# Kernel optimization log

Measured on AMD Instinct MI355X. Metric: run time of the kernel, lower is better.

## Reference

```python
import jax, jax.numpy as jnp
import numpy as np

BN_EPS = 1e-5
LEAKY_SLOPE = 0.2


def setup_inputs() -> dict:
    key = jax.random.key(0)
    k1, k2 = jax.random.split(key, 2)
    B, C, N, O, K = 8, 64, 4096, 64, 20
    x = jax.random.normal(k1, (B, C, N), dtype=jnp.float32)
    W = jax.random.normal(k2, (O, 2 * C), dtype=jnp.float32) * 0.05  # 1x1 conv weight
    gamma = jnp.ones((O,), dtype=jnp.float32)
    beta = jnp.zeros((O,), dtype=jnp.float32)
    return {"x": x, "W": W, "gamma": gamma, "beta": beta, "k": K}


def reference(x, W, gamma, beta, k):
    # x: (B, C, N)
    xt = jnp.transpose(x, (0, 2, 1))  # (B, N, C)
    # kNN via squared euclidean distances (same ordering as cdist p=2)
    sq = jnp.sum(xt * xt, axis=-1)  # (B, N)
    d2 = sq[:, :, None] + sq[:, None, :] - 2.0 * jnp.einsum('bnc,bmc->bnm', xt, xt)
    idx = jax.lax.top_k(-d2, k)[1]  # (B, N, k) nearest neighbors (incl. self)
    # gather neighbor features: (B, N, k, C)
    xj = jax.vmap(lambda f, i: f[i])(xt, idx)
    xi = xt[:, :, None, :]  # (B, N, 1, C)
    edge = jnp.concatenate([xj - xi, jnp.broadcast_to(xi, xj.shape)], axis=-1)  # (B, N, k, 2C)
    # 1x1 conv == channel GEMM
    h = jnp.einsum('bnkc,oc->bnko', edge, W)  # (B, N, k, O)
    # BatchNorm2d, training-mode batch statistics over (B, N, k) per channel
    mean = jnp.mean(h, axis=(0, 1, 2))
    var = jnp.mean(jnp.square(h - mean), axis=(0, 1, 2))
    hn = (h - mean) * jax.lax.rsqrt(var + BN_EPS) * gamma + beta
    # LeakyReLU(0.2); dropout omitted (eval / identity)
    act = jnp.where(hn >= 0, hn, LEAKY_SLOPE * hn)
    # max over the k neighbors -> (B, N, O) -> (B, O, N)
    out = jnp.max(act, axis=2)
    return jnp.transpose(out, (0, 2, 1))
```

## Files before the change

### kernel.cpp

```cpp
#include <hip/hip_runtime.h>
#include <math.h>

#define Bn 8
#define Cc 64
#define Nn 4096
#define Oo 64
#define Kk 20
#define Kh 10
#define QCAP 32
#define NTOT (Bn*Nn*Kk)

typedef __attribute__((ext_vector_type(8))) short short8;
typedef __attribute__((ext_vector_type(4))) float f32x4;

__device__ __forceinline__ unsigned bf16_rn(float v) {
  unsigned u = __float_as_uint(v);
  return (u + 0x7FFFu + ((u >> 16) & 1)) >> 16;
}

__device__ __forceinline__ float pair_swap_f(float v) {
  return __int_as_float(__builtin_amdgcn_mov_dpp(__float_as_int(v), 0xB1, 0xF, 0xF, true));
}
__device__ __forceinline__ int pair_swap_i(int v) {
  return __builtin_amdgcn_mov_dpp(v, 0xB1, 0xF, 0xF, true);
}

__device__ __forceinline__ void gload_lds16(const void* g, void* l) {
  __builtin_amdgcn_global_load_lds((const __attribute__((address_space(1))) void*)g,
                                   (__attribute__((address_space(3))) void*)l,
                                   16, 0, 0);
}

__global__ __launch_bounds__(256) void k_split(const float* __restrict__ x,
                                               unsigned short* __restrict__ xs3,
                                               float* __restrict__ sqv) {
  __shared__ float xs[64][68];
  int tid = threadIdx.x;
  int b = blockIdx.x & 7;
  int n0 = (blockIdx.x >> 3) << 6;
  for (int i = 0; i < 4; i++) {
    int c = i * 16 + (tid >> 4);
    int n = (tid & 15) * 4;
    float4 v = *(const float4*)&x[((size_t)b * Cc + c) * Nn + n0 + n];
    *(float4*)&xs[c][n] = v;
  }
  __syncthreads();
  for (int i = 0; i < 4; i++) {
    int n = i * 16 + (tid >> 4);
    int c = (tid & 15) * 4;
    ushort4 h4, m4, l4;
    unsigned short* hp = (unsigned short*)&h4;
    unsigned short* mp = (unsigned short*)&m4;
    unsigned short* lp = (unsigned short*)&l4;
#pragma unroll
    for (int j = 0; j < 4; j++) {
      float v = xs[c + j][n];
      unsigned hb = bf16_rn(v);
      float hf = __uint_as_float(hb << 16);
      float r1 = v - hf;
      unsigned mb = bf16_rn(r1);
      float mf = __uint_as_float(mb << 16);
      float r2 = r1 - mf;
      unsigned lb = bf16_rn(r2);
      hp[j] = (unsigned short)hb;
      mp[j] = (unsigned short)mb;
      lp[j] = (unsigned short)lb;
    }
    size_t o = ((size_t)(b << 12) + n0 + n) * 192 + c;
    *(ushort4*)&xs3[o] = h4;
    *(ushort4*)&xs3[o + 64] = m4;
    *(ushort4*)&xs3[o + 128] = l4;
  }
  if (tid < 64) {
    float s = 0.f;
#pragma unroll
    for (int c = 0; c < 64; c++) { float v = xs[c][tid]; s = fmaf(v, v, s); }
    sqv[b * Nn + n0 + tid] = s;
  }
}

__global__ __launch_bounds__(256) void k_y1z(const float* __restrict__ x,
                                             const float* __restrict__ Wm,
                                             float* __restrict__ y1,
                                             float* __restrict__ z) {
  __shared__ float xs[64][68];
  __shared__ float Wl[64][129];
  int tid = threadIdx.x;
  int b = blockIdx.x & 7;
  int n0 = (blockIdx.x >> 3) << 6;
  for (int i = tid; i < 64 * 128; i += 256) Wl[i >> 7][i & 127] = Wm[i];
  for (int i = 0; i < 4; i++) {
    int c = i * 16 + (tid >> 4);
    int n = (tid & 15) * 4;
    float4 v = *(const float4*)&x[((size_t)b * Cc + c) * Nn + n0 + n];
    *(float4*)&xs[c][n] = v;
  }
  __syncthreads();
  int o = tid & 63, ng = tid >> 6;
  for (int p = 0; p < 4; p++) {
    int nb = p * 16 + ng * 4;
    float a1[4] = {0.f, 0.f, 0.f, 0.f};
    float a2[4] = {0.f, 0.f, 0.f, 0.f};
#pragma unroll 8
    for (int c = 0; c < 64; c++) {
      float4 xv = *(const float4*)&xs[c][nb];
      float w1v = Wl[o][c], w2v = Wl[o][64 + c];
      float xa[4] = {xv.x, xv.y, xv.z, xv.w};
#pragma unroll
      for (int j = 0; j < 4; j++) {
        a1[j] = fmaf(xa[j], w1v, a1[j]);
        a2[j] = fmaf(xa[j], w2v, a2[j]);
      }
    }
#pragma unroll
    for (int j = 0; j < 4; j++) {
      size_t off = ((size_t)b * Nn + n0 + nb + j) * 64 + o;
      y1[off] = a1[j];
      z[off] = a2[j] - a1[j];
    }
  }
}

__global__ __launch_bounds__(512, 4) void k_knn(const unsigned short* __restrict__ xs3,
                                                const float* __restrict__ sqv,
                                                int* __restrict__ idxout) {
  __shared__ alignas(16) short Bs[2][2][6144];
  __shared__ alignas(16) float thrS[2][64];
  __shared__ alignas(16) float sqs[2][2][32];
  __shared__ alignas(16) float qk[2][64][36];
  __shared__ alignas(16) unsigned short qm[2][64][40];
  __shared__ int qcnt[2][64];

  const int tid = threadIdx.x;
  const int lane = tid & 63;
  const int w = tid >> 6;
  const int grp = w >> 2;
  const int wg = w & 3;
  const int tig = tid & 255;
  const int b = blockIdx.x & 7;
  const int n0 = (blockIdx.x >> 3) << 6;
  const int lm = lane & 15;
  const int q = lane >> 4;
  const bool handler = (lane < 32);
  const int hrow = wg * 16 + (lane >> 1);
  const bool isL = (lane & 1) == 0;
  const int rowq = wg * 16 + q * 4;

  float hk[Kh];
  int hix[Kh];
#pragma unroll
  for (int kk = 0; kk < Kh; kk++) { hk[kk] = INFINITY; hix[kk] = 0; }

  if (handler && !isL) { thrS[grp][hrow] = INFINITY; qcnt[grp][hrow] = 0; }

  const size_t arow = ((size_t)(b << 12) + n0 + wg * 16 + lm) * 192;
  short8 ah0 = *(const short8*)&xs3[arow + q * 8];
  short8 ah1 = *(const short8*)&xs3[arow + 32 + q * 8];
  short8 am0 = *(const short8*)&xs3[arow + 64 + q * 8];
  short8 am1 = *(const short8*)&xs3[arow + 96 + q * 8];
  short8 al0 = *(const short8*)&xs3[arow + 128 + q * 8];
  short8 al1 = *(const short8*)&xs3[arow + 160 + q * 8];

  const unsigned short* gbase = xs3 + ((size_t)(b << 12) + grp * 2048) * 192;
  int gofs[3];
  int lofs[3];
#pragma unroll
  for (int i = 0; i < 3; i++) {
    int p = i * 256 + wg * 64 + lane;
    gofs[i] = (p ^ ((p / 24) & 7)) * 8;
    lofs[i] = (i * 256 + wg * 64) * 8;
  }
  const int qa = ((q ^ (lm & 7)) << 3);
  const int qb = (((q + 4) ^ (lm & 7)) << 3);

#pragma unroll
  for (int i = 0; i < 3; i++) gload_lds16(gbase + gofs[i], &Bs[grp][0][lofs[i]]);
  if (tig < 8) gload_lds16(sqv + b * Nn + grp * 2048 + lane * 4, &sqs[grp][0][0]);

  int cur = 0;
  for (int t = 0; t < 64; t++) {
    const int m0 = grp * 2048 + t * 32;
    __syncthreads();
    if (t < 63) {
      const unsigned short* gn = gbase + 6144;
#pragma unroll
      for (int i = 0; i < 3; i++) gload_lds16(gn + gofs[i], &Bs[grp][cur ^ 1][lofs[i]]);
      if (tig < 8) gload_lds16(sqv + b * Nn + m0 + 32 + lane * 4, &sqs[grp][cur ^ 1][0]);
      gbase = gn;
    }

    const short* Bg = &Bs[grp][cur][0];
    f32x4 acc[2];
#pragma unroll
    for (int g = 0; g < 2; g++) {
      const short* brow = Bg + (g * 16 + lm) * 192;
      short8 bh0 = *(const short8*)(brow + qa);
      short8 bh1 = *(const short8*)(brow + qb);
      short8 bm0 = *(const short8*)(brow + 64 + qa);
      short8 bm1 = *(const short8*)(brow + 64 + qb);
      short8 bl0 = *(const short8*)(brow + 128 + qa);
      short8 bl1 = *(const short8*)(brow + 128 + qb);
      f32x4 a = (f32x4){0.f, 0.f, 0.f, 0.f};
      a = __builtin_amdgcn_mfma_f32_16x16x32_bf16(am0, bm0, a, 0, 0, 0);
      a = __builtin_amdgcn_mfma_f32_16x16x32_bf16(am1, bm1, a, 0, 0, 0);
      a = __builtin_amdgcn_mfma_f32_16x16x32_bf16(ah0, bl0, a, 0, 0, 0);
      a = __builtin_amdgcn_mfma_f32_16x16x32_bf16(ah1, bl1, a, 0, 0, 0);
      a = __builtin_amdgcn_mfma_f32_16x16x32_bf16(al0, bh0, a, 0, 0, 0);
      a = __builtin_amdgcn_mfma_f32_16x16x32_bf16(al1, bh1, a, 0, 0, 0);
      a = __builtin_amdgcn_mfma_f32_16x16x32_bf16(ah0, bm0, a, 0, 0, 0);
      a = __builtin_amdgcn_mfma_f32_16x16x32_bf16(ah1, bm1, a, 0, 0, 0);
      a = __builtin_amdgcn_mfma_f32_16x16x32_bf16(am0, bh0, a, 0, 0, 0);
      a = __builtin_amdgcn_mfma_f32_16x16x32_bf16(am1, bh1, a, 0, 0, 0);
      a = __builtin_amdgcn_mfma_f32_16x16x32_bf16(ah0, bh0, a, 0, 0, 0);
      a = __builtin_amdgcn_mfma_f32_16x16x32_bf16(ah1, bh1, a, 0, 0, 0);
      acc[g] = a;
    }

    unsigned pend = 0;
    {
      float4 t4 = *(const float4*)&thrS[grp][rowq];
      float tl[4] = {t4.x, t4.y, t4.z, t4.w};
      if (grp) {
        float4 s4 = *(const float4*)&thrS[0][rowq];
        tl[0] = fminf(tl[0], s4.x); tl[1] = fminf(tl[1], s4.y);
        tl[2] = fminf(tl[2], s4.z); tl[3] = fminf(tl[3], s4.w);
      }
#pragma unroll
      for (int g = 0; g < 2; g++) {
        float sv = sqs[grp][cur][g * 16 + lm];
#pragma unroll
        for (int r = 0; r < 4; r++) {
          float key = fmaf(-2.f, acc[g][r], sv);
          acc[g][r] = key;
          if (key < tl[r]) pend |= 1u << (g * 4 + r);
        }
      }
    }

    if (pend) {
#pragma unroll
      for (int g = 0; g < 2; g++) {
#pragma unroll
        for (int r = 0; r < 4; r++) {
          unsigned bit = 1u << (g * 4 + r);
          if (pend & bit) {
            int row = rowq + r;
            int p = atomicAdd(&qcnt[grp][row], 1);
            qk[grp][row][p] = acc[g][r];
            qm[grp][row][p] = (unsigned short)(m0 + g * 16 + lm);
          }
        }
      }
    }

    if (handler) {
      int cn = qcnt[grp][hrow];
      for (int p0 = 0; p0 < cn; p0 += 2) {
        float2 kv2 = *(const float2*)&qk[grp][hrow][p0];
        ushort2 mv2 = *(const ushort2*)&qm[grp][hrow][p0];
        float kva[2] = {kv2.x, kv2.y};
        unsigned short mva[2] = {mv2.x, mv2.y};
#pragma unroll
        for (int j = 0; j < 2; j++) {
          bool valid = (p0 + j < cn);
          float kv = kva[j];
          int ki = (int)mva[j];
          bool lins = kv < hk[Kh - 1];
          float pv_ = lins ? hk[Kh - 1] : kv;
          int pi_ = lins ? hix[Kh - 1] : ki;
          float rv = pair_swap_f(pv_);
          int ri = pair_swap_i(pi_);
          float mval = isL ? kv : rv;
          int midx = isL ? ki : ri;
          if (valid && mval < hk[Kh - 1]) {
            bool cm[Kh];
#pragma unroll
            for (int kk = 0; kk < Kh; kk++) cm[kk] = mval < hk[kk];
#pragma unroll
            for (int kk = Kh - 1; kk >= 1; kk--) {
              hk[kk]  = cm[kk] ? (cm[kk - 1] ? hk[kk - 1]  : mval) : hk[kk];
              hix[kk] = cm[kk] ? (cm[kk - 1] ? hix[kk - 1] : midx) : hix[kk];
            }
            if (cm[0]) { hk[0] = mval; hix[0] = midx; }
          }
        }
      }
      if (cn && !isL) { qcnt[grp][hrow] = 0; thrS[grp][hrow] = hk[Kh - 1]; }
    }
    cur ^= 1;
  }

  if (grp == 1 && handler) {
    int base = isL ? 0 : Kh;
#pragma unroll
    for (int kk = 0; kk < Kh; kk++) {
      qk[1][hrow][base + kk] = hk[kk];
      qm[1][hrow][base + kk] = (unsigned short)hix[kk];
    }
  }
  __syncthreads();
  if (grp == 0 && handler) {
    for (int p0 = 0; p0 < Kk; p0 += 4) {
      float4 kv4 = *(const float4*)&qk[1][hrow][p0];
      ushort4 mv4 = *(const ushort4*)&qm[1][hrow][p0];
      float kva[4] = {kv4.x, kv4.y, kv4.z, kv4.w};
      unsigned short mva[4] = {mv4.x, mv4.y, mv4.z, mv4.w};
#pragma unroll
      for (int j = 0; j < 4; j++) {
        float kv = kva[j];
        int ki = (int)mva[j];
        bool lins = kv < hk[Kh - 1];
        float pv_ = lins ? hk[Kh - 1] : kv;
        int pi_ = lins ? hix[Kh - 1] : ki;
        float rv = pair_swap_f(pv_);
        int ri = pair_swap_i(pi_);
        float mval = isL ? kv : rv;
        int midx = isL ? ki : ri;
        if (mval < hk[Kh - 1]) {
          bool cm[Kh];
#pragma unroll
          for (int kk = 0; kk < Kh; kk++) cm[kk] = mval < hk[kk];
#pragma unroll
          for (int kk = Kh - 1; kk >= 1; kk--) {
            hk[kk]  = cm[kk] ? (cm[kk - 1] ? hk[kk - 1]  : mval) : hk[kk];
            hix[kk] = cm[kk] ? (cm[kk - 1] ? hix[kk - 1] : midx) : hix[kk];
          }
          if (cm[0]) { hk[0] = mval; hix[0] = midx; }
        }
      }
    }
    size_t obase = ((size_t)b * Nn + n0 + hrow) * Kk + (isL ? 0 : Kh);
#pragma unroll
    for (int kk = 0; kk < Kh; kk++) idxout[obase + kk] = hix[kk];
  }
}

__global__ __launch_bounds__(256) void k_stats(const float* __restrict__ y1,
                                               const float* __restrict__ z,
                                               const int* __restrict__ idxp,
                                               float* __restrict__ parts) {
  __shared__ float rs[4][64];
  __shared__ float rq[4][64];
  int tid = threadIdx.x;
  int o = tid & 63, g = tid >> 6;
  int b = blockIdx.x & 7;
  int n0 = (blockIdx.x >> 3) << 6;
  const float* y1b = y1 + (size_t)b * Nn * 64;
  float s = 0.f, ss = 0.f;
  for (int t = 0; t < 16; t++) {
    int n = n0 + g + t * 4;
    size_t base = (size_t)b * Nn + n;
    float zv = z[base * 64 + o];
    const int* ip = idxp + base * Kk;
#pragma unroll
    for (int k = 0; k < Kk; k++) {
      int j = ip[k];
      float hv = y1b[(size_t)j * 64 + o] + zv;
      s += hv;
      ss = fmaf(hv, hv, ss);
    }
  }
  rs[g][o] = s;
  rq[g][o] = ss;
  __syncthreads();
  if (tid < 64) {
    parts[(size_t)blockIdx.x * 128 + tid] = rs[0][tid] + rs[1][tid] + rs[2][tid] + rs[3][tid];
    parts[(size_t)blockIdx.x * 128 + 64 + tid] = rq[0][tid] + rq[1][tid] + rq[2][tid] + rq[3][tid];
  }
}

__global__ __launch_bounds__(128) void k_reduce(const float* __restrict__ parts,
                                                float* __restrict__ stats) {
  int tid = threadIdx.x;
  float s = 0.f;
  for (int i = 0; i < 512; i += 4) {
    s += parts[(size_t)i * 128 + tid] + parts[(size_t)(i + 1) * 128 + tid] +
         parts[(size_t)(i + 2) * 128 + tid] + parts[(size_t)(i + 3) * 128 + tid];
  }
  stats[tid] = s;
}

__global__ __launch_bounds__(256) void k_out(const float* __restrict__ y1,
                                             const float* __restrict__ z,
                                             const int* __restrict__ idxp,
                                             const float* __restrict__ stats,
                                             const float* __restrict__ gamma,
                                             const float* __restrict__ beta,
                                             float* __restrict__ out) {
  __shared__ float T[64][65];
  int tid = threadIdx.x;
  int lane = tid & 63;
  int w = tid >> 6;
  int b = blockIdx.x & 7;
  int n0 = (blockIdx.x >> 3) << 6;
  int o = lane;
  const float inv = 1.0f / (float)NTOT;
  float mean = stats[o] * inv;
  float var = fmaf(-mean, mean, stats[64 + o] * inv);
  float sc = gamma[o] * rsqrtf(var + 1e-5f);
  float bi = fmaf(-mean, sc, beta[o]);
  const float* y1b = y1 + (size_t)b * Nn * 64;
  for (int t = 0; t < 16; t++) {
    int nl = w + t * 4;
    size_t base = (size_t)b * Nn + n0 + nl;
    float zv = z[base * 64 + o];
    const int* ip = idxp + base * Kk;
    float mv = -INFINITY;
#pragma unroll
    for (int k = 0; k < Kk; k++) {
      int j = ip[k];
      float hv = y1b[(size_t)j * 64 + o] + zv;
      float hn = fmaf(hv, sc, bi);
      float a = (hn >= 0.f) ? hn : 0.2f * hn;
      mv = fmaxf(mv, a);
    }
    T[o][nl] = mv;
  }
  __syncthreads();
  for (int t = 0; t < 16; t++) {
    int oo = w * 16 + t;
    out[((size_t)b * Oo + oo) * Nn + n0 + lane] = T[oo][lane];
  }
}

extern "C" void kernel_launch(void* const* d_in, const int* in_sizes, int n_in,
                              void* d_out, int out_size, void* d_ws, size_t ws_size,
                              hipStream_t stream) {
  const float* x = (const float*)d_in[0];
  const float* W = (const float*)d_in[1];
  const float* gamma = (const float*)d_in[2];
  const float* beta = (const float*)d_in[3];

  char* ws = (char*)d_ws;
  unsigned short* xs3 = (unsigned short*)ws;
  float* y1 = (float*)ws;
  float* z = (float*)(ws + 8388608);
  float* sq = (float*)(ws + 16777216);
  float* stats = (float*)(ws + 16908288);
  int* idx = (int*)(ws + 16908800);
  float* parts = (float*)(ws + 19530240);
  float* out = (float*)d_out;

  k_split<<<Bn * (Nn / 64), 256, 0, stream>>>(x, xs3, sq);
  k_knn<<<Bn * (Nn / 64), 512, 0, stream>>>(xs3, sq, idx);
  k_y1z<<<Bn * (Nn / 64), 256, 0, stream>>>(x, W, y1, z);
  k_stats<<<Bn * (Nn / 64), 256, 0, stream>>>(y1, z, idx, parts);
  k_reduce<<<1, 128, 0, stream>>>(parts, stats);
  k_out<<<Bn * (Nn / 64), 256, 0, stream>>>(y1, z, idx, stats, gamma, beta, out);
}
```

Baseline: 366.6 us.

## Precompute per-point max/min of pre-BN features to avoid second neighbor gather

The stats kernel now also records the max and min of the pre-normalization feature over the k neighbors for each point and channel, writing them transposed (hmax into the output buffer, hmin into workspace). Because BN followed by LeakyReLU is monotonic in each channel (direction set by the sign of the scale), the output kernel only needs an elementwise transform of max or min instead of a second 20-way gather. The kNN candidate filter also changes: each group now tests against the other group's threshold too, with tie-breaking asymmetry, which may cut queue insertions. In exchange there are extra stores and shared memory in the stats kernel, plus an in-place read/write of the output buffer.

```diff
diff --git a/kernel.cpp b/kernel.cpp
--- a/kernel.cpp
+++ b/kernel.cpp
@@ -219,12 +219,9 @@
     unsigned pend = 0;
     {
       float4 t4 = *(const float4*)&thrS[grp][rowq];
+      float4 u4 = *(const float4*)&thrS[grp ^ 1][rowq];
       float tl[4] = {t4.x, t4.y, t4.z, t4.w};
-      if (grp) {
-        float4 s4 = *(const float4*)&thrS[0][rowq];
-        tl[0] = fminf(tl[0], s4.x); tl[1] = fminf(tl[1], s4.y);
-        tl[2] = fminf(tl[2], s4.z); tl[3] = fminf(tl[3], s4.w);
-      }
+      float ul[4] = {u4.x, u4.y, u4.z, u4.w};
 #pragma unroll
       for (int g = 0; g < 2; g++) {
         float sv = sqs[grp][cur][g * 16 + lm];
@@ -232,7 +229,8 @@
         for (int r = 0; r < 4; r++) {
           float key = fmaf(-2.f, acc[g][r], sv);
           acc[g][r] = key;
-          if (key < tl[r]) pend |= 1u << (g * 4 + r);
+          bool keep = (key < tl[r]) && (grp ? (key < ul[r]) : (key <= ul[r]));
+          if (keep) pend |= 1u << (g * 4 + r);
         }
       }
     }
@@ -338,9 +336,13 @@
 __global__ __launch_bounds__(256) void k_stats(const float* __restrict__ y1,
                                                const float* __restrict__ z,
                                                const int* __restrict__ idxp,
-                                               float* __restrict__ parts) {
+                                               float* __restrict__ parts,
+                                               float* __restrict__ hmax,
+                                               float* __restrict__ hmin) {
   __shared__ float rs[4][64];
   __shared__ float rq[4][64];
+  __shared__ float Tmx[64][65];
+  __shared__ float Tmn[64][65];
   int tid = threadIdx.x;
   int o = tid & 63, g = tid >> 6;
   int b = blockIdx.x & 7;
@@ -348,17 +350,23 @@
   const float* y1b = y1 + (size_t)b * Nn * 64;
   float s = 0.f, ss = 0.f;
   for (int t = 0; t < 16; t++) {
-    int n = n0 + g + t * 4;
+    int nl = g + t * 4;
+    int n = n0 + nl;
     size_t base = (size_t)b * Nn + n;
     float zv = z[base * 64 + o];
     const int* ip = idxp + base * Kk;
+    float mx = -INFINITY, mn = INFINITY;
 #pragma unroll
     for (int k = 0; k < Kk; k++) {
       int j = ip[k];
       float hv = y1b[(size_t)j * 64 + o] + zv;
       s += hv;
       ss = fmaf(hv, hv, ss);
-    }
+      mx = fmaxf(mx, hv);
+      mn = fminf(mn, hv);
+    }
+    Tmx[o][nl] = mx;
+    Tmn[o][nl] = mn;
   }
   rs[g][o] = s;
   rq[g][o] = ss;
@@ -366,6 +374,13 @@
   if (tid < 64) {
     parts[(size_t)blockIdx.x * 128 + tid] = rs[0][tid] + rs[1][tid] + rs[2][tid] + rs[3][tid];
     parts[(size_t)blockIdx.x * 128 + 64 + tid] = rq[0][tid] + rq[1][tid] + rq[2][tid] + rq[3][tid];
+  }
+  int lane = tid & 63;
+  for (int t = 0; t < 16; t++) {
+    int oo = g * 16 + t;
+    size_t ob = ((size_t)b * Oo + oo) * Nn + n0 + lane;
+    hmax[ob] = Tmx[oo][lane];
+    hmin[ob] = Tmn[oo][lane];
   }
 }
 
@@ -380,47 +395,32 @@
   stats[tid] = s;
 }
 
-__global__ __launch_bounds__(256) void k_out(const float* __restrict__ y1,
-                                             const float* __restrict__ z,
-                                             const int* __restrict__ idxp,
+__global__ __launch_bounds__(256) void k_out(const float* __restrict__ hmax,
+                                             const float* __restrict__ hmin,
                                              const float* __restrict__ stats,
                                              const float* __restrict__ gamma,
                                              const float* __restrict__ beta,
                                              float* __restrict__ out) {
-  __shared__ float T[64][65];
-  int tid = threadIdx.x;
-  int lane = tid & 63;
-  int w = tid >> 6;
-  int b = blockIdx.x & 7;
-  int n0 = (blockIdx.x >> 3) << 6;
-  int o = lane;
+  int idx4 = blockIdx.x * 256 + threadIdx.x;
+  int o = (idx4 >> 10) & 63;
   const float inv = 1.0f / (float)NTOT;
   float mean = stats[o] * inv;
   float var = fmaf(-mean, mean, stats[64 + o] * inv);
   float sc = gamma[o] * rsqrtf(var + 1e-5f);
   float bi = fmaf(-mean, sc, beta[o]);
-  const float* y1b = y1 + (size_t)b * Nn * 64;
-  for (int t = 0; t < 16; t++) {
-    int nl = w + t * 4;
-    size_t base = (size_t)b * Nn + n0 + nl;
-    float zv = z[base * 64 + o];
-    const int* ip = idxp + base * Kk;
-    float mv = -INFINITY;
-#pragma unroll
-    for (int k = 0; k < Kk; k++) {
-      int j = ip[k];
-      float hv = y1b[(size_t)j * 64 + o] + zv;
-      float hn = fmaf(hv, sc, bi);
-      float a = (hn >= 0.f) ? hn : 0.2f * hn;
-      mv = fmaxf(mv, a);
-    }
-    T[o][nl] = mv;
-  }
-  __syncthreads();
-  for (int t = 0; t < 16; t++) {
-    int oo = w * 16 + t;
-    out[((size_t)b * Oo + oo) * Nn + n0 + lane] = T[oo][lane];
-  }
+  float4 mx = ((const float4*)hmax)[idx4];
+  float4 mn = ((const float4*)hmin)[idx4];
+  float mxa[4] = {mx.x, mx.y, mx.z, mx.w};
+  float mna[4] = {mn.x, mn.y, mn.z, mn.w};
+  float4 r;
+  float* rp = (float*)&r;
+#pragma unroll
+  for (int j = 0; j < 4; j++) {
+    float v = (sc >= 0.f) ? mxa[j] : mna[j];
+    float hn = fmaf(v, sc, bi);
+    rp[j] = (hn >= 0.f) ? hn : 0.2f * hn;
+  }
+  ((float4*)out)[idx4] = r;
 }
 
 extern "C" void kernel_launch(void* const* d_in, const int* in_sizes, int n_in,
@@ -439,12 +439,13 @@
   float* stats = (float*)(ws + 16908288);
   int* idx = (int*)(ws + 16908800);
   float* parts = (float*)(ws + 19530240);
+  float* hmin = (float*)(ws + 19792384);
   float* out = (float*)d_out;
 
   k_split<<<Bn * (Nn / 64), 256, 0, stream>>>(x, xs3, sq);
   k_knn<<<Bn * (Nn / 64), 512, 0, stream>>>(xs3, sq, idx);
   k_y1z<<<Bn * (Nn / 64), 256, 0, stream>>>(x, W, y1, z);
-  k_stats<<<Bn * (Nn / 64), 256, 0, stream>>>(y1, z, idx, parts);
+  k_stats<<<Bn * (Nn / 64), 256, 0, stream>>>(y1, z, idx, parts, out, hmin);
   k_reduce<<<1, 128, 0, stream>>>(parts, stats);
-  k_out<<<Bn * (Nn / 64), 256, 0, stream>>>(y1, z, idx, stats, gamma, beta, out);
-}
+  k_out<<<Bn * Oo * Nn / 1024, 256, 0, stream>>>(out, hmin, stats, gamma, beta, out);
+}
```

Measured after the change: 357.4 us. 1.03x faster.
